# Kernel optimization log

Measured on AMD Instinct MI355X. Metric: run time of the kernel, lower is better.

## Reference

```python
import jax, jax.numpy as jnp
import numpy as np

B, N, DIM, HID = 32, 10000, 64, 128


def _linear_params(key, fan_in, fan_out):
    kw, kb = jax.random.split(key)
    bound = 1.0 / np.sqrt(fan_in)
    w = jax.random.uniform(kw, (fan_out, fan_in), jnp.float32, -bound, bound)
    b = jax.random.uniform(kb, (fan_out,), jnp.float32, -bound, bound)
    return w, b


def setup_inputs() -> dict:
    key = jax.random.key(0)
    ks = jax.random.split(key, 7)
    x = jax.random.normal(ks[0], (B, N, DIM), jnp.float32)
    adj_col = jax.random.uniform(ks[1], (N,), jnp.float32)
    n2e_w, n2e_b = _linear_params(ks[2], 2 * DIM, HID)
    e2e_w, e2e_b = _linear_params(ks[3], HID, HID)
    e2n_w, e2n_b = _linear_params(ks[4], HID, HID)
    n2n_w, n2n_b = _linear_params(ks[5], HID, HID)
    out_w, out_b = _linear_params(ks[6], DIM + HID, DIM)
    return {
        "x": x, "adj_col": adj_col,
        "n2e_w": n2e_w, "n2e_b": n2e_b,
        "e2e_w": e2e_w, "e2e_b": e2e_b,
        "e2n_w": e2n_w, "e2n_b": e2n_b,
        "n2n_w": n2n_w, "n2n_b": n2n_b,
        "out_w": out_w, "out_b": out_b,
        "i": 5, "num": 4, "node_size": 2000,
    }


def reference(x, adj_col, n2e_w, n2e_b, e2e_w, e2e_b, e2n_w, e2n_b,
              n2n_w, n2n_b, out_w, out_b, i, num, node_size):
    # The torch loop over (num+1) chunks is an execution tiling; mathematically it
    # computes a full sum over all N nodes. We vectorize it in one pass.
    starter = x[:, i, :]                                   # [B, dim]
    ender = jnp.broadcast_to(starter[:, None, :], x.shape)  # [B, N, dim]
    c = jnp.concatenate([x, ender], axis=-1)               # [B, N, 2*dim]
    h = jax.nn.relu(jnp.einsum('bnd,hd->bnh', c, n2e_w) + n2e_b)
    h = jax.nn.relu(jnp.einsum('bnh,gh->bng', h, e2e_w) + e2e_b)
    h = h * adj_col[None, :, None]                         # adjacency mask
    s = jnp.sum(h, axis=1)                                 # [B, hid]
    y = jax.nn.relu(s @ e2n_w.T + e2n_b)
    y = jax.nn.relu(y @ n2n_w.T + n2n_b)
    out = jnp.concatenate([starter, y], axis=-1) @ out_w.T + out_b  # [B, dim]
    return out
```

## Files before the change

### kernel.cpp

```cpp
#include <hip/hip_runtime.h>
#include <hip/hip_bf16.h>

typedef float f32x4 __attribute__((ext_vector_type(4)));
typedef short bf16x8 __attribute__((ext_vector_type(8)));
typedef unsigned short u16;
typedef unsigned int u32;

#define NB 32
#define NN 10000
#define DIMX 64

__device__ __forceinline__ u16 f2bf(float f) {
    union { float f; unsigned u; } v; v.f = f;
    unsigned r = (v.u + 0x7FFFu + ((v.u >> 16) & 1u)) >> 16;
    return (u16)r;
}

__device__ __forceinline__ u32 pkbf(float a, float b) {
    __hip_bfloat162 h = __float22bfloat162_rn(make_float2(a, b));
    u32 r; __builtin_memcpy(&r, &h, 4); return r;
}

__global__ void k_prep(const float* __restrict__ x, const float* __restrict__ n2e_w,
                       const float* __restrict__ n2e_b, const float* __restrict__ e2e_w,
                       const int* __restrict__ ip,
                       float* __restrict__ bias1, u16* __restrict__ w1p, u16* __restrict__ w2p) {
    int id = blockIdx.x * 256 + threadIdx.x;
    if (id < 4096) {
        int b = id >> 7, j = id & 127;
        int i = ip[0];
        const float* xr = x + ((size_t)b * NN + i) * DIMX;
        const float* w = n2e_w + j * 128 + 64;
        float s = n2e_b[j];
        #pragma unroll
        for (int d = 0; d < 64; ++d) s += xr[d] * w[d];
        bias1[b * 128 + j] = s;
    } else if (id < 12288) {
        int e = id - 4096;
        int i8 = e & 7, lane = (e >> 3) & 63, kk = (e >> 9) & 1, t = e >> 10;
        int row = t * 16 + (lane & 15), col = kk * 32 + (lane >> 4) * 8 + i8;
        w1p[e] = f2bf(n2e_w[row * 128 + col]);
    } else if (id < 28672) {
        int e = id - 12288;
        int i8 = e & 7, lane = (e >> 3) & 63, kk = (e >> 9) & 3, t = e >> 11;
        int row = t * 16 + (lane & 15), col = kk * 32 + (lane >> 4) * 8 + i8;
        w2p[e] = f2bf(e2e_w[row * 128 + col]);
    }
}

__global__ __launch_bounds__(256, 3) void k_main(
        const float* __restrict__ x, const float* __restrict__ adj,
        const float* __restrict__ bias1, const u16* __restrict__ w1p,
        const u16* __restrict__ w2p, const float* __restrict__ e2e_b,
        float* __restrict__ partials) {
    __shared__ u16 sW1[8192];
    __shared__ u16 sH1[16384];
    __shared__ float sBias[256];

    const int tid = threadIdx.x;
    const int lane = tid & 63, wave = tid >> 6;
    const int c = lane & 15, g = lane >> 4;
    const int bid = blockIdx.x;
    const int b = bid / 24, qb = bid - b * 24;
    const int s0 = qb ? 27 + (qb - 1) * 26 : 0;
    const int cnt = qb ? 26 : 27;

    #pragma unroll
    for (int p = 0; p < 4; ++p) { int o = (p * 256 + tid) * 8;
        *(bf16x8*)&sW1[o] = *(const bf16x8*)&w1p[o]; }
    if (tid < 128) sBias[tid] = bias1[b * 128 + tid];
    else if (tid < 256) sBias[tid] = e2e_b[tid - 128];

    const bf16x8* const gW2 = (const bf16x8*)w2p;
    bf16x8 w2r[2][4];
    #pragma unroll
    for (int tt = 0; tt < 2; ++tt)
        #pragma unroll
        for (int kk2 = 0; kk2 < 4; ++kk2)
            w2r[tt][kk2] = gW2[((wave * 2 + tt) * 4 + kk2) * 64 + lane];

    float sAcc[2] = {0.f, 0.f};
    __syncthreads();

    const size_t xbatch = (size_t)b * NN;
    const int swzW = 16 * (c & 3);
    const int rdOff = (c * 64 + 16 * (g ^ (c & 3))) >> 1;

    f32x4 xl[4];
    {
        int idx = wave;
        int stl = idx < cnt ? idx : cnt - 1;
        const float* xr = x + (xbatch + (s0 + stl) * 16 + c) * 64 + g * 8;
        xl[0] = *(const f32x4*)(xr);
        xl[1] = *(const f32x4*)(xr + 4);
        xl[2] = *(const f32x4*)(xr + 32);
        xl[3] = *(const f32x4*)(xr + 36);
    }

    int par = 0;
    #pragma unroll 1
    for (int it = 0; it < 7; ++it) {
        bf16x8 A1[2];
        #pragma unroll
        for (int kk = 0; kk < 2; ++kk) {
            f32x4 lo = xl[kk * 2], hi = xl[kk * 2 + 1];
            union { bf16x8 v; u32 w[4]; } u;
            u.w[0] = pkbf(lo[0], lo[1]); u.w[1] = pkbf(lo[2], lo[3]);
            u.w[2] = pkbf(hi[0], hi[1]); u.w[3] = pkbf(hi[2], hi[3]);
            A1[kk] = u.v;
        }
        if (it < 6) {
            int idx = (it + 1) * 4 + wave;
            int stl = idx < cnt ? idx : cnt - 1;
            const float* xr = x + (xbatch + (s0 + stl) * 16 + c) * 64 + g * 8;
            xl[0] = *(const f32x4*)(xr);
            xl[1] = *(const f32x4*)(xr + 4);
            xl[2] = *(const f32x4*)(xr + 32);
            xl[3] = *(const f32x4*)(xr + 36);
        }

        u16* const bufW = &sH1[par * 8192 + wave * 512];
        #pragma unroll
        for (int kk2 = 0; kk2 < 4; ++kk2) {
            const int t0 = kk2 * 2, t1 = kk2 * 2 + 1;
            bf16x8 w1a0 = *(const bf16x8*)&sW1[(t0 * 2 + 0) * 512 + lane * 8];
            bf16x8 w1b0 = *(const bf16x8*)&sW1[(t0 * 2 + 1) * 512 + lane * 8];
            bf16x8 w1a1 = *(const bf16x8*)&sW1[(t1 * 2 + 0) * 512 + lane * 8];
            bf16x8 w1b1 = *(const bf16x8*)&sW1[(t1 * 2 + 1) * 512 + lane * 8];
            f32x4 cb0 = *(const f32x4*)&sBias[t0 * 16 + 4 * g];
            f32x4 cb1 = *(const f32x4*)&sBias[t1 * 16 + 4 * g];
            f32x4 d0 = __builtin_amdgcn_mfma_f32_16x16x32_bf16(w1a0, A1[0], cb0, 0, 0, 0);
            d0 = __builtin_amdgcn_mfma_f32_16x16x32_bf16(w1b0, A1[1], d0, 0, 0, 0);
            f32x4 d1 = __builtin_amdgcn_mfma_f32_16x16x32_bf16(w1a1, A1[0], cb1, 0, 0, 0);
            d1 = __builtin_amdgcn_mfma_f32_16x16x32_bf16(w1b1, A1[1], d1, 0, 0, 0);
            u32 p00 = pkbf(fmaxf(d0[0], 0.f), fmaxf(d0[1], 0.f));
            u32 p01 = pkbf(fmaxf(d0[2], 0.f), fmaxf(d0[3], 0.f));
            u32 p10 = pkbf(fmaxf(d1[0], 0.f), fmaxf(d1[1], 0.f));
            u32 p11 = pkbf(fmaxf(d1[2], 0.f), fmaxf(d1[3], 0.f));
            int base = c * 64;
            *(uint2*)&bufW[kk2 * 2048 + ((base + ((8 * g) ^ swzW)) >> 1)]      = make_uint2(p00, p01);
            *(uint2*)&bufW[kk2 * 2048 + ((base + ((32 + 8 * g) ^ swzW)) >> 1)] = make_uint2(p10, p11);
        }
        __syncthreads();

        f32x4 acc[4][2];
        #pragma unroll
        for (int sub = 0; sub < 4; ++sub)
            #pragma unroll
            for (int tt = 0; tt < 2; ++tt) acc[sub][tt] = (f32x4){0.f,0.f,0.f,0.f};
        const u16* const bufR = &sH1[par * 8192];
        #pragma unroll
        for (int kk2 = 0; kk2 < 4; ++kk2) {
            bf16x8 A2[4];
            #pragma unroll
            for (int sub = 0; sub < 4; ++sub)
                A2[sub] = *(const bf16x8*)&bufR[kk2 * 2048 + sub * 512 + rdOff];
            #pragma unroll
            for (int tt = 0; tt < 2; ++tt)
                #pragma unroll
                for (int sub = 0; sub < 4; ++sub)
                    acc[sub][tt] = __builtin_amdgcn_mfma_f32_16x16x32_bf16(A2[sub], w2r[tt][kk2], acc[sub][tt], 0, 0, 0);
        }

        f32x4 adjv[4];
        #pragma unroll
        for (int sub = 0; sub < 4; ++sub) {
            int idx = it * 4 + sub;
            if (idx < cnt) adjv[sub] = *(const f32x4*)(adj + (s0 + idx) * 16 + 4 * g);
            else adjv[sub] = (f32x4){0.f,0.f,0.f,0.f};
        }
        #pragma unroll
        for (int tt = 0; tt < 2; ++tt) {
            float bb = sBias[128 + (wave * 2 + tt) * 16 + c];
            #pragma unroll
            for (int sub = 0; sub < 4; ++sub)
                #pragma unroll
                for (int r = 0; r < 4; ++r)
                    sAcc[tt] = fmaf(adjv[sub][r], fmaxf(acc[sub][tt][r] + bb, 0.f), sAcc[tt]);
        }
        par ^= 1;
    }

    float red[2];
    #pragma unroll
    for (int tt = 0; tt < 2; ++tt) {
        float v = sAcc[tt];
        v += __shfl_xor(v, 16, 64);
        v += __shfl_xor(v, 32, 64);
        red[tt] = v;
    }
    if (lane < 16) {
        #pragma unroll
        for (int tt = 0; tt < 2; ++tt)
            partials[bid * 128 + (wave * 2 + tt) * 16 + lane] = red[tt];
    }
}

__global__ void k_final(const float* __restrict__ partials, const float* __restrict__ x,
                        const int* __restrict__ ip,
                        const float* __restrict__ e2n_w, const float* __restrict__ e2n_b,
                        const float* __restrict__ n2n_w, const float* __restrict__ n2n_b,
                        const float* __restrict__ out_w, const float* __restrict__ out_b,
                        float* __restrict__ out) {
    int b = blockIdx.x, j = threadIdx.x;
    __shared__ float s0[128], s1[128], s2[128];
    float acc = 0.f;
    #pragma unroll
    for (int qq = 0; qq < 24; ++qq) acc += partials[(b * 24 + qq) * 128 + j];
    s0[j] = acc;
    __syncthreads();
    {
        float a1 = e2n_b[j];
        const float* w = e2n_w + j * 128;
        #pragma unroll 8
        for (int k = 0; k < 128; ++k) a1 += w[k] * s0[k];
        s1[j] = fmaxf(a1, 0.f);
    }
    __syncthreads();
    {
        float a2 = n2n_b[j];
        const float* w = n2n_w + j * 128;
        #pragma unroll 8
        for (int k = 0; k < 128; ++k) a2 += w[k] * s1[k];
        s2[j] = fmaxf(a2, 0.f);
    }
    __syncthreads();
    if (j < 64) {
        int i = ip[0];
        const float* xr = x + ((size_t)b * NN + i) * DIMX;
        const float* ow = out_w + j * 192;
        float o = out_b[j];
        #pragma unroll 8
        for (int m = 0; m < 64; ++m) o += ow[m] * xr[m];
        #pragma unroll 8
        for (int m = 0; m < 128; ++m) o += ow[64 + m] * s2[m];
        out[b * 64 + j] = o;
    }
}

extern "C" void kernel_launch(void* const* d_in, const int* in_sizes, int n_in,
                              void* d_out, int out_size, void* d_ws, size_t ws_size,
                              hipStream_t stream) {
    const float* x      = (const float*)d_in[0];
    const float* adj    = (const float*)d_in[1];
    const float* n2e_w  = (const float*)d_in[2];
    const float* n2e_b  = (const float*)d_in[3];
    const float* e2e_w  = (const float*)d_in[4];
    const float* e2e_b  = (const float*)d_in[5];
    const float* e2n_w  = (const float*)d_in[6];
    const float* e2n_b  = (const float*)d_in[7];
    const float* n2n_w  = (const float*)d_in[8];
    const float* n2n_b  = (const float*)d_in[9];
    const float* out_w  = (const float*)d_in[10];
    const float* out_b  = (const float*)d_in[11];
    const int*   ip     = (const int*)d_in[12];
    float* out = (float*)d_out;

    char* ws = (char*)d_ws;
    float* bias1    = (float*)ws;
    u16*   w1p      = (u16*)(ws + 16384);
    u16*   w2p      = (u16*)(ws + 32768);
    float* partials = (float*)(ws + 65536);

    k_prep<<<112, 256, 0, stream>>>(x, n2e_w, n2e_b, e2e_w, ip, bias1, w1p, w2p);
    k_main<<<768, 256, 0, stream>>>(x, adj, bias1, w1p, w2p, e2e_b, partials);
    k_final<<<32, 128, 0, stream>>>(partials, x, ip, e2n_w, e2n_b, n2n_w, n2n_b,
                                    out_w, out_b, out);
}
```

Before: 46.99 us.

## Fuse prep, main and final kernels into one with last-block reduction

Removes the separate prep and final kernels. Each block now converts the fp32 weights to bf16 and computes the per-batch bias itself, and the last block to finish for each batch, found through an atomic counter, runs the small MLP tail. Adjacency values are staged in shared memory instead of being loaded per iteration. This cuts two kernel launches and their serialization, but every block repeats the weight conversion and bias dot product, and a memset is added before the launch.

```diff
diff --git a/kernel.cpp b/kernel.cpp
--- a/kernel.cpp
+++ b/kernel.cpp
@@ -10,52 +10,26 @@
 #define NN 10000
 #define DIMX 64
 
-__device__ __forceinline__ u16 f2bf(float f) {
-    union { float f; unsigned u; } v; v.f = f;
-    unsigned r = (v.u + 0x7FFFu + ((v.u >> 16) & 1u)) >> 16;
-    return (u16)r;
-}
-
 __device__ __forceinline__ u32 pkbf(float a, float b) {
     __hip_bfloat162 h = __float22bfloat162_rn(make_float2(a, b));
     u32 r; __builtin_memcpy(&r, &h, 4); return r;
 }
 
-__global__ void k_prep(const float* __restrict__ x, const float* __restrict__ n2e_w,
-                       const float* __restrict__ n2e_b, const float* __restrict__ e2e_w,
-                       const int* __restrict__ ip,
-                       float* __restrict__ bias1, u16* __restrict__ w1p, u16* __restrict__ w2p) {
-    int id = blockIdx.x * 256 + threadIdx.x;
-    if (id < 4096) {
-        int b = id >> 7, j = id & 127;
-        int i = ip[0];
-        const float* xr = x + ((size_t)b * NN + i) * DIMX;
-        const float* w = n2e_w + j * 128 + 64;
-        float s = n2e_b[j];
-        #pragma unroll
-        for (int d = 0; d < 64; ++d) s += xr[d] * w[d];
-        bias1[b * 128 + j] = s;
-    } else if (id < 12288) {
-        int e = id - 4096;
-        int i8 = e & 7, lane = (e >> 3) & 63, kk = (e >> 9) & 1, t = e >> 10;
-        int row = t * 16 + (lane & 15), col = kk * 32 + (lane >> 4) * 8 + i8;
-        w1p[e] = f2bf(n2e_w[row * 128 + col]);
-    } else if (id < 28672) {
-        int e = id - 12288;
-        int i8 = e & 7, lane = (e >> 3) & 63, kk = (e >> 9) & 3, t = e >> 11;
-        int row = t * 16 + (lane & 15), col = kk * 32 + (lane >> 4) * 8 + i8;
-        w2p[e] = f2bf(e2e_w[row * 128 + col]);
-    }
-}
-
-__global__ __launch_bounds__(256, 3) void k_main(
+__global__ __launch_bounds__(256, 3) void k_fused(
         const float* __restrict__ x, const float* __restrict__ adj,
-        const float* __restrict__ bias1, const u16* __restrict__ w1p,
-        const u16* __restrict__ w2p, const float* __restrict__ e2e_b,
-        float* __restrict__ partials) {
+        const float* __restrict__ n2e_w, const float* __restrict__ n2e_b,
+        const float* __restrict__ e2e_w, const float* __restrict__ e2e_b,
+        const float* __restrict__ e2n_w, const float* __restrict__ e2n_b,
+        const float* __restrict__ n2n_w, const float* __restrict__ n2n_b,
+        const float* __restrict__ out_w, const float* __restrict__ out_b,
+        const int* __restrict__ ip,
+        float* __restrict__ partials, int* __restrict__ ctr,
+        float* __restrict__ out) {
     __shared__ u16 sW1[8192];
     __shared__ u16 sH1[16384];
     __shared__ float sBias[256];
+    __shared__ float sAdj[448];
+    __shared__ int sLast;
 
     const int tid = threadIdx.x;
     const int lane = tid & 63, wave = tid >> 6;
@@ -64,20 +38,46 @@
     const int b = bid / 24, qb = bid - b * 24;
     const int s0 = qb ? 27 + (qb - 1) * 26 : 0;
     const int cnt = qb ? 26 : 27;
+    const int i0 = ip[0];
 
     #pragma unroll
-    for (int p = 0; p < 4; ++p) { int o = (p * 256 + tid) * 8;
-        *(bf16x8*)&sW1[o] = *(const bf16x8*)&w1p[o]; }
-    if (tid < 128) sBias[tid] = bias1[b * 128 + tid];
-    else if (tid < 256) sBias[tid] = e2e_b[tid - 128];
-
-    const bf16x8* const gW2 = (const bf16x8*)w2p;
+    for (int p = 0; p < 4; ++p) {
+        int fp = p * 256 + tid;
+        int f = fp >> 6, ln = fp & 63;
+        int t = f >> 1, kk = f & 1;
+        int row = t * 16 + (ln & 15), col = kk * 32 + (ln >> 4) * 8;
+        const float* src = n2e_w + row * 128 + col;
+        f32x4 lo = *(const f32x4*)src, hi = *(const f32x4*)(src + 4);
+        union { bf16x8 v; u32 w[4]; } u;
+        u.w[0] = pkbf(lo[0], lo[1]); u.w[1] = pkbf(lo[2], lo[3]);
+        u.w[2] = pkbf(hi[0], hi[1]); u.w[3] = pkbf(hi[2], hi[3]);
+        *(bf16x8*)&sW1[fp * 8] = u.v;
+    }
     bf16x8 w2r[2][4];
     #pragma unroll
     for (int tt = 0; tt < 2; ++tt)
         #pragma unroll
-        for (int kk2 = 0; kk2 < 4; ++kk2)
-            w2r[tt][kk2] = gW2[((wave * 2 + tt) * 4 + kk2) * 64 + lane];
+        for (int kk2 = 0; kk2 < 4; ++kk2) {
+            int row = (wave * 2 + tt) * 16 + c, col = kk2 * 32 + g * 8;
+            const float* src = e2e_w + row * 128 + col;
+            f32x4 lo = *(const f32x4*)src, hi = *(const f32x4*)(src + 4);
+            union { bf16x8 v; u32 w[4]; } u;
+            u.w[0] = pkbf(lo[0], lo[1]); u.w[1] = pkbf(lo[2], lo[3]);
+            u.w[2] = pkbf(hi[0], hi[1]); u.w[3] = pkbf(hi[2], hi[3]);
+            w2r[tt][kk2] = u.v;
+        }
+    if (tid < 128) {
+        const float* xr = x + ((size_t)b * NN + i0) * DIMX;
+        const float* w = n2e_w + tid * 128 + 64;
+        float s = n2e_b[tid];
+        #pragma unroll 16
+        for (int d = 0; d < 64; ++d) s += xr[d] * w[d];
+        sBias[tid] = s;
+    } else {
+        sBias[tid] = e2e_b[tid - 128];
+    }
+    for (int idx = tid; idx < 448; idx += 256)
+        sAdj[idx] = (idx < cnt * 16) ? adj[s0 * 16 + idx] : 0.f;
 
     float sAcc[2] = {0.f, 0.f};
     __syncthreads();
@@ -162,21 +162,16 @@
                     acc[sub][tt] = __builtin_amdgcn_mfma_f32_16x16x32_bf16(A2[sub], w2r[tt][kk2], acc[sub][tt], 0, 0, 0);
         }
 
-        f32x4 adjv[4];
-        #pragma unroll
-        for (int sub = 0; sub < 4; ++sub) {
-            int idx = it * 4 + sub;
-            if (idx < cnt) adjv[sub] = *(const f32x4*)(adj + (s0 + idx) * 16 + 4 * g);
-            else adjv[sub] = (f32x4){0.f,0.f,0.f,0.f};
-        }
         #pragma unroll
         for (int tt = 0; tt < 2; ++tt) {
             float bb = sBias[128 + (wave * 2 + tt) * 16 + c];
             #pragma unroll
-            for (int sub = 0; sub < 4; ++sub)
+            for (int sub = 0; sub < 4; ++sub) {
+                f32x4 av = *(const f32x4*)&sAdj[(it * 4 + sub) * 16 + 4 * g];
                 #pragma unroll
                 for (int r = 0; r < 4; ++r)
-                    sAcc[tt] = fmaf(adjv[sub][r], fmaxf(acc[sub][tt][r] + bb, 0.f), sAcc[tt]);
+                    sAcc[tt] = fmaf(av[r], fmaxf(acc[sub][tt][r] + bb, 0.f), sAcc[tt]);
+            }
         }
         par ^= 1;
     }
@@ -194,47 +189,49 @@
         for (int tt = 0; tt < 2; ++tt)
             partials[bid * 128 + (wave * 2 + tt) * 16 + lane] = red[tt];
     }
-}
-
-__global__ void k_final(const float* __restrict__ partials, const float* __restrict__ x,
-                        const int* __restrict__ ip,
-                        const float* __restrict__ e2n_w, const float* __restrict__ e2n_b,
-                        const float* __restrict__ n2n_w, const float* __restrict__ n2n_b,
-                        const float* __restrict__ out_w, const float* __restrict__ out_b,
-                        float* __restrict__ out) {
-    int b = blockIdx.x, j = threadIdx.x;
-    __shared__ float s0[128], s1[128], s2[128];
-    float acc = 0.f;
-    #pragma unroll
-    for (int qq = 0; qq < 24; ++qq) acc += partials[(b * 24 + qq) * 128 + j];
-    s0[j] = acc;
-    __syncthreads();
-    {
-        float a1 = e2n_b[j];
-        const float* w = e2n_w + j * 128;
-        #pragma unroll 8
-        for (int k = 0; k < 128; ++k) a1 += w[k] * s0[k];
-        s1[j] = fmaxf(a1, 0.f);
-    }
-    __syncthreads();
-    {
-        float a2 = n2n_b[j];
-        const float* w = n2n_w + j * 128;
-        #pragma unroll 8
-        for (int k = 0; k < 128; ++k) a2 += w[k] * s1[k];
-        s2[j] = fmaxf(a2, 0.f);
-    }
-    __syncthreads();
-    if (j < 64) {
-        int i = ip[0];
-        const float* xr = x + ((size_t)b * NN + i) * DIMX;
-        const float* ow = out_w + j * 192;
-        float o = out_b[j];
+
+    __threadfence();
+    if (tid == 0) {
+        int prev = atomicAdd(&ctr[b], 1);
+        sLast = (prev == 23);
+    }
+    __syncthreads();
+    if (!sLast) return;
+    __threadfence();
+
+    float* sF = (float*)sH1;
+    if (tid < 128) {
+        float a0 = 0.f;
+        #pragma unroll
+        for (int qq = 0; qq < 24; ++qq) a0 += partials[(b * 24 + qq) * 128 + tid];
+        sF[tid] = a0;
+    }
+    __syncthreads();
+    if (tid < 128) {
+        float a1 = e2n_b[tid];
+        const float* w = e2n_w + tid * 128;
+        #pragma unroll 8
+        for (int k = 0; k < 128; ++k) a1 += w[k] * sF[k];
+        sF[128 + tid] = fmaxf(a1, 0.f);
+    }
+    __syncthreads();
+    if (tid < 128) {
+        float a2 = n2n_b[tid];
+        const float* w = n2n_w + tid * 128;
+        #pragma unroll 8
+        for (int k = 0; k < 128; ++k) a2 += w[k] * sF[128 + k];
+        sF[256 + tid] = fmaxf(a2, 0.f);
+    }
+    __syncthreads();
+    if (tid < 64) {
+        const float* xr = x + ((size_t)b * NN + i0) * DIMX;
+        const float* ow = out_w + tid * 192;
+        float o = out_b[tid];
         #pragma unroll 8
         for (int m = 0; m < 64; ++m) o += ow[m] * xr[m];
         #pragma unroll 8
-        for (int m = 0; m < 128; ++m) o += ow[64 + m] * s2[m];
-        out[b * 64 + j] = o;
+        for (int m = 0; m < 128; ++m) o += ow[64 + m] * sF[256 + m];
+        out[b * 64 + tid] = o;
     }
 }
 
@@ -257,13 +254,11 @@
     float* out = (float*)d_out;
 
     char* ws = (char*)d_ws;
-    float* bias1    = (float*)ws;
-    u16*   w1p      = (u16*)(ws + 16384);
-    u16*   w2p      = (u16*)(ws + 32768);
-    float* partials = (float*)(ws + 65536);
-
-    k_prep<<<112, 256, 0, stream>>>(x, n2e_w, n2e_b, e2e_w, ip, bias1, w1p, w2p);
-    k_main<<<768, 256, 0, stream>>>(x, adj, bias1, w1p, w2p, e2e_b, partials);
-    k_final<<<32, 128, 0, stream>>>(partials, x, ip, e2n_w, e2n_b, n2n_w, n2n_b,
-                                    out_w, out_b, out);
+    int*   ctr      = (int*)ws;
+    float* partials = (float*)(ws + 512);
+
+    hipMemsetAsync(ctr, 0, 32 * sizeof(int), stream);
+    k_fused<<<768, 256, 0, stream>>>(x, adj, n2e_w, n2e_b, e2e_w, e2e_b,
+                                     e2n_w, e2n_b, n2n_w, n2n_b, out_w, out_b,
+                                     ip, partials, ctr, out);
 }
```

Result: slower. 130.3 us (+177.3%).
